# Kernel tuning notes

Hardware: AMD Instinct MI355X
Metric: run time of the kernel (lower is better)

## Reference

```python
import jax, jax.numpy as jnp
import numpy as np

B, T, S, D, V, NX = 4, 256, 400, 512, 50000, 50
VEXT = V + NX  # extended vocab


def setup_inputs() -> dict:
    key = jax.random.key(0)
    ks = jax.random.split(key, 10)
    s = 0.02
    return {
        "x": jax.random.normal(ks[0], (B, T, D), dtype=jnp.float32),
        "enc_outputs": jax.random.normal(ks[1], (B, S, D), dtype=jnp.float32),
        "src_mask": jax.random.randint(ks[2], (B, 1, S), 0, 2, dtype=jnp.int32),
        "enc_batch_extend_vocab": jax.random.randint(ks[3], (B, S), 0, VEXT, dtype=jnp.int64),
        "extra_zeros": jnp.zeros((B, T, NX), dtype=jnp.float32),
        "fc_w": jax.random.normal(ks[4], (V, D), dtype=jnp.float32) * s,
        "fc_b": jnp.zeros((V,), dtype=jnp.float32),
        "pgen_w": jax.random.normal(ks[5], (1, D), dtype=jnp.float32) * s,
        "pgen_b": jnp.zeros((1,), dtype=jnp.float32),
        "wq": jax.random.normal(ks[6], (D, D), dtype=jnp.float32) * s,
        "bq": jnp.zeros((D,), dtype=jnp.float32),
        "wk": jax.random.normal(ks[7], (D, D), dtype=jnp.float32) * s,
        "bk": jnp.zeros((D,), dtype=jnp.float32),
    }


def reference(x, enc_outputs, src_mask, enc_batch_extend_vocab, extra_zeros,
              fc_w, fc_b, pgen_w, pgen_b, wq, bq, wk, bk):
    # vocab distribution: [B,T,V]
    p_vocab = jax.nn.softmax(x @ fc_w.T + fc_b, axis=-1)
    # single-head cross attention probs (h=1 -> d_k = D)
    q = x @ wq.T + bq                 # [B,T,D]
    k = enc_outputs @ wk.T + bk       # [B,S,D]
    scores = jnp.einsum('btd,bsd->bts', q, k) / jnp.sqrt(jnp.float32(D))
    scores = jnp.where(src_mask == 0, jnp.float32(-1e9), scores)  # mask [B,1,S]
    attn_probs = jax.nn.softmax(scores, axis=-1)  # [B,T,S]
    # generation gate
    p_gen = jax.nn.sigmoid(x @ pgen_w.T + pgen_b)  # [B,T,1]
    attn_dist = (1.0 - p_gen) * attn_probs         # copy distribution over source
    p_ext = jnp.concatenate([p_gen * p_vocab, extra_zeros], axis=-1)  # [B,T,VEXT]
    # scatter-add copy probs into extended vocab slots
    b_idx = jnp.arange(B)[:, None, None]
    t_idx = jnp.arange(T)[None, :, None]
    v_idx = enc_batch_extend_vocab[:, None, :]
    bb, tt, vv = jnp.broadcast_arrays(b_idx, t_idx, v_idx)  # each [B,T,S]
    p_ext = p_ext.at[bb, tt, vv].add(attn_dist)
    return jnp.log(jnp.maximum(p_ext, jnp.float32(1e-9)))
```

## Files before the change

kernel.cpp:

```cpp
#include <hip/hip_runtime.h>
#include <hip/hip_bf16.h>
#include <math.h>

constexpr int cB = 4, cT = 256, cS = 400, cD = 512, cV = 50000, cNX = 50;
constexpr int cVEXT = cV + cNX;
constexpr int cPAN  = (cV + 127) / 128;
constexpr int cCBLD = cVEXT * 2;
constexpr int cMQ   = cB * cT;

typedef __attribute__((ext_vector_type(8))) short short8v;
typedef __attribute__((ext_vector_type(4))) float floatx4;

__device__ inline ushort f2bf(float f) {
    union { float f; unsigned u; } v; v.f = f;
    unsigned r = (v.u + 0x7FFFu + ((v.u >> 16) & 1u)) >> 16;
    return (ushort)r;
}
__device__ inline float bf2f(ushort u) {
    union { unsigned u; float f; } v; v.u = ((unsigned)u) << 16;
    return v.f;
}

__global__ __launch_bounds__(256) void cast_kernel(
    const float* __restrict__ src, ushort* __restrict__ dst, int n4)
{
    const int stride = gridDim.x * 256;
    for (int i = blockIdx.x * 256 + threadIdx.x; i < n4; i += stride) {
        float4 v = *(const float4*)(src + (size_t)i * 4);
        ushort4 o;
        o.x = f2bf(v.x); o.y = f2bf(v.y); o.z = f2bf(v.z); o.w = f2bf(v.w);
        *(ushort4*)(dst + (size_t)i * 4) = o;
    }
}

template<bool STATS>
__global__ __launch_bounds__(256) void gemm2(
    const ushort* __restrict__ A, const ushort* __restrict__ Wb,
    const float* __restrict__ bias,
    float* __restrict__ Cf, ushort* __restrict__ Cb, int cbld,
    float* __restrict__ pm, float* __restrict__ ps,
    int M, int N, int K, int ldc)
{
    __shared__ ushort As[2][128 * 32];
    __shared__ ushort Bs[2][128 * 32];
    __shared__ float sm_m[2][128];
    __shared__ float sm_s[2][128];

    const int tid  = threadIdx.x;
    const int lane = tid & 63;
    const int wv   = tid >> 6;
    const int wm   = wv >> 1;
    const int wn   = wv & 1;

    int bm, bn, pan = 0;
    if constexpr (STATS) {
        const int wg  = blockIdx.y * gridDim.x + blockIdx.x;
        const int nwg = gridDim.x * gridDim.y;
        const int j   = (wg & 7) * (nwg >> 3) + (wg >> 3);
        pan = j >> 3;
        bm  = (j & 7) * 128;
        bn  = pan * 128;
    } else {
        bm = blockIdx.x * 128;
        bn = blockIdx.y * 128;
    }

    const int srow = lane >> 2;
    const int sk   = (lane & 3) * 8;

    const int nt = K >> 5;

    floatx4 acc[4][4] = {};

    auto stage = [&](int bidx, int t) {
        const int k0 = t * 32;
        #pragma unroll
        for (int c = 0; c < 2; ++c) {
            const int lr = wv * 32 + c * 16;
            int ga = bm + lr + srow; if (ga >= M) ga = M - 1;
            __builtin_amdgcn_global_load_lds(
                (const __attribute__((address_space(1))) void*)(A + (size_t)ga * K + k0 + sk),
                (__attribute__((address_space(3))) void*)&As[bidx][lr * 32], 16, 0, 0);
        }
        #pragma unroll
        for (int c = 0; c < 2; ++c) {
            const int lr = wv * 32 + c * 16;
            int gb = bn + lr + srow; if (gb >= N) gb = N - 1;
            __builtin_amdgcn_global_load_lds(
                (const __attribute__((address_space(1))) void*)(Wb + (size_t)gb * K + k0 + sk),
                (__attribute__((address_space(3))) void*)&Bs[bidx][lr * 32], 16, 0, 0);
        }
    };

    stage(0, 0);
    __syncthreads();

    const int fr = lane & 15;
    const int g  = lane >> 4;
    int buf = 0;

    for (int t = 0; t < nt; ++t) {
        if (t + 1 < nt) stage(buf ^ 1, t + 1);
        short8v a[4], b[4];
        #pragma unroll
        for (int mi = 0; mi < 4; ++mi)
            a[mi] = *(const short8v*)&As[buf][(wm * 64 + mi * 16 + fr) * 32 + g * 8];
        #pragma unroll
        for (int ni = 0; ni < 4; ++ni)
            b[ni] = *(const short8v*)&Bs[buf][(wn * 64 + ni * 16 + fr) * 32 + g * 8];
        #pragma unroll
        for (int mi = 0; mi < 4; ++mi)
            #pragma unroll
            for (int ni = 0; ni < 4; ++ni)
                acc[mi][ni] = __builtin_amdgcn_mfma_f32_16x16x32_bf16(
                    a[mi], b[ni], acc[mi][ni], 0, 0, 0);
        __syncthreads();
        buf ^= 1;
    }

    float bv[4]; bool val[4];
    #pragma unroll
    for (int ni = 0; ni < 4; ++ni) {
        const int colg = bn + wn * 64 + ni * 16 + fr;
        val[ni] = (colg < N);
        bv[ni] = val[ni] ? bias[colg] : 0.f;
    }
    #pragma unroll
    for (int mi = 0; mi < 4; ++mi)
        #pragma unroll
        for (int ni = 0; ni < 4; ++ni)
            #pragma unroll
            for (int r = 0; r < 4; ++r)
                acc[mi][ni][r] += bv[ni];

    if constexpr (STATS) {
        #pragma unroll
        for (int mi = 0; mi < 4; ++mi) {
            #pragma unroll
            for (int r = 0; r < 4; ++r) {
                float mx = -1e30f;
                #pragma unroll
                for (int ni = 0; ni < 4; ++ni)
                    if (val[ni]) mx = fmaxf(mx, acc[mi][ni][r]);
                #pragma unroll
                for (int sw = 1; sw < 16; sw <<= 1)
                    mx = fmaxf(mx, __shfl_xor(mx, sw));
                float sm = 0.f;
                #pragma unroll
                for (int ni = 0; ni < 4; ++ni)
                    if (val[ni]) sm += __expf(acc[mi][ni][r] - mx);
                #pragma unroll
                for (int sw = 1; sw < 16; sw <<= 1)
                    sm += __shfl_xor(sm, sw);
                if (fr == 0) {
                    const int rl = wm * 64 + mi * 16 + g * 4 + r;
                    sm_m[wn][rl] = mx;
                    sm_s[wn][rl] = sm;
                }
            }
        }
        __syncthreads();
        if (tid < 128) {
            const float m0 = sm_m[0][tid], m1 = sm_m[1][tid];
            const float s0 = sm_s[0][tid], s1 = sm_s[1][tid];
            const float mm = fmaxf(m0, m1);
            const float ss = s0 * __expf(m0 - mm) + s1 * __expf(m1 - mm);
            const int grow = bm + tid;
            if (grow < M) {
                pm[(size_t)pan * M + grow] = mm;
                ps[(size_t)pan * M + grow] = ss;
            }
        }
        #pragma unroll
        for (int mi = 0; mi < 4; ++mi) {
            #pragma unroll
            for (int ni = 0; ni < 4; ++ni) {
                if (!val[ni]) continue;
                const int colg = bn + wn * 64 + ni * 16 + fr;
                #pragma unroll
                for (int r = 0; r < 4; ++r) {
                    const int row = bm + wm * 64 + mi * 16 + g * 4 + r;
                    if (row < M) Cb[(size_t)row * cbld + colg] = f2bf(acc[mi][ni][r]);
                }
            }
        }
    } else {
        #pragma unroll
        for (int mi = 0; mi < 4; ++mi) {
            #pragma unroll
            for (int ni = 0; ni < 4; ++ni) {
                if (!val[ni]) continue;
                const int colg = bn + wn * 64 + ni * 16 + fr;
                #pragma unroll
                for (int r = 0; r < 4; ++r) {
                    const int row = bm + wm * 64 + mi * 16 + g * 4 + r;
                    if (row < M) Cf[(size_t)row * ldc + colg] = acc[mi][ni][r];
                }
            }
        }
    }
}

__global__ __launch_bounds__(256) void combine_kernel(
    const float* __restrict__ pm, const float* __restrict__ ps,
    const float* __restrict__ pgen, float* __restrict__ rowadd)
{
    const int row = blockIdx.x;
    const int tid = threadIdx.x;
    float m = -1e30f, s = 0.f;
    for (int i = tid; i < cPAN; i += 256) {
        const float mi = pm[(size_t)i * cMQ + row];
        const float si = ps[(size_t)i * cMQ + row];
        const float nm = fmaxf(m, mi);
        s = s * __expf(m - nm) + si * __expf(mi - nm);
        m = nm;
    }
    #pragma unroll
    for (int sw = 1; sw < 64; sw <<= 1) {
        const float mo = __shfl_xor(m, sw);
        const float so = __shfl_xor(s, sw);
        const float nm = fmaxf(m, mo);
        s = s * __expf(m - nm) + so * __expf(mo - nm);
        m = nm;
    }
    __shared__ float rm[4], rs[4];
    if ((tid & 63) == 0) { rm[tid >> 6] = m; rs[tid >> 6] = s; }
    __syncthreads();
    if (tid == 0) {
        m = rm[0]; s = rs[0];
        #pragma unroll
        for (int i = 1; i < 4; ++i) {
            const float nm = fmaxf(m, rm[i]);
            s = s * __expf(m - nm) + rs[i] * __expf(rm[i] - nm);
            m = nm;
        }
        rowadd[row] = __logf(pgen[row]) - m - __logf(s);
    }
}

__global__ __launch_bounds__(512) void transform_flat(
    float* __restrict__ out, const ushort* __restrict__ lb,
    const float* __restrict__ rowadd)
{
    const int row = blockIdx.y;
    const float a = rowadd[row];
    constexpr float LOGMIN = -20.72326583694641f;
    const ushort* src = lb + (size_t)row * cV;
    float* dst = out + (size_t)row * cVEXT;
    constexpr int NI = cV / 8;
    for (int i = blockIdx.x * 512 + threadIdx.x; i <= NI; i += gridDim.x * 512) {
        if (i < NI) {
            const short8v sv = *(const short8v*)(src + (size_t)i * 8);
            const int v = i * 8;
            #pragma unroll
            for (int j = 0; j < 4; ++j) {
                float2 o;
                o.x = fmaxf(bf2f((ushort)sv[2 * j])     + a, LOGMIN);
                o.y = fmaxf(bf2f((ushort)sv[2 * j + 1]) + a, LOGMIN);
                *(float2*)&dst[v + 2 * j] = o;
            }
        } else {
            #pragma unroll
            for (int v = cV; v < cVEXT; v += 2) {
                float2 o; o.x = LOGMIN; o.y = LOGMIN;
                *(float2*)&dst[v] = o;
            }
        }
    }
}

__global__ __launch_bounds__(256) void fixup_kernel(
    float* __restrict__ out, const int* __restrict__ ebev,
    const float* __restrict__ attn)
{
    const int row = blockIdx.x;
    const int b = row / cT;
    const int tid = threadIdx.x;
    __shared__ int   pos[cS];
    __shared__ float add[cS];
    for (int s = tid; s < cS; s += 256) {
        pos[s] = ebev[b * cS + s];
        add[s] = attn[(size_t)row * cS + s];
    }
    __syncthreads();
    float* rowf = out + (size_t)row * cVEXT;
    for (int s = tid; s < cS; s += 256) {
        const int p = pos[s];
        bool leader = true;
        for (int s2 = 0; s2 < s; ++s2)
            if (pos[s2] == p) { leader = false; break; }
        if (!leader) continue;
        float sum = add[s];
        for (int s2 = s + 1; s2 < cS; ++s2)
            if (pos[s2] == p) sum += add[s2];
        const float base = __expf(rowf[p]);
        rowf[p] = __logf(fmaxf(base + sum, 1e-9f));
    }
}

__global__ __launch_bounds__(512) void transform_inplace(
    float* __restrict__ out, const float* __restrict__ rowadd,
    const int* __restrict__ ebev, const float* __restrict__ attn)
{
    const int row = blockIdx.x;
    const int b   = row / cT;
    const int tid = threadIdx.x;
    constexpr float LOGMIN = -20.72326583694641f;

    __shared__ int   pos[cS];
    __shared__ float add[cS];
    for (int s = tid; s < cS; s += 512) {
        pos[s] = ebev[b * cS + s];
        add[s] = attn[(size_t)row * cS + s];
    }

    const float a = rowadd[row];
    ushort* rowu = (ushort*)out + (size_t)row * cCBLD;
    float*  rowf = out + (size_t)row * cVEXT;

    #pragma unroll 1
    for (int L = 32768; L >= 2; L >>= 1) {
        const int hi = (2 * L < cVEXT) ? 2 * L : cVEXT;
        for (int i = L + 2 * tid; i < hi; i += 1024) {
            const float x0 = bf2f(rowu[i]);
            const float x1 = bf2f(rowu[i + 1]);
            float2 o;
            o.x = (i     < cV) ? fmaxf(x0 + a, LOGMIN) : LOGMIN;
            o.y = (i + 1 < cV) ? fmaxf(x1 + a, LOGMIN) : LOGMIN;
            *(float2*)&rowf[i] = o;
        }
        __syncthreads();
    }
    if (tid == 0) {
        const float x1 = bf2f(rowu[1]);
        const float x0 = bf2f(rowu[0]);
        rowf[1] = fmaxf(x1 + a, LOGMIN);
        rowf[0] = fmaxf(x0 + a, LOGMIN);
    }
    __syncthreads();

    for (int s = tid; s < cS; s += 512) {
        const int p = pos[s];
        bool leader = true;
        for (int s2 = 0; s2 < s; ++s2)
            if (pos[s2] == p) { leader = false; break; }
        if (!leader) continue;
        float sum = add[s];
        for (int s2 = s + 1; s2 < cS; ++s2)
            if (pos[s2] == p) sum += add[s2];
        const float base = __expf(rowf[p]);
        rowf[p] = __logf(fmaxf(base + sum, 1e-9f));
    }
}

__global__ __launch_bounds__(64) void pgen_kernel(
    const float* __restrict__ x, const float* __restrict__ w,
    const float* __restrict__ b, float* __restrict__ pgen)
{
    const int row = blockIdx.x;
    const int lane = threadIdx.x;
    const float* xr = x + (size_t)row * cD;
    float s = 0.f;
    for (int i = lane; i < cD; i += 64) s += xr[i] * w[i];
    #pragma unroll
    for (int off = 32; off; off >>= 1) s += __shfl_down(s, off);
    if (lane == 0) pgen[row] = 1.f / (1.f + __expf(-(s + b[0])));
}

__global__ __launch_bounds__(256) void attn_kernel(
    const float* __restrict__ q, const float* __restrict__ k,
    const int* __restrict__ src_mask, const float* __restrict__ pgen,
    float* __restrict__ attn)
{
    constexpr float scale = 0.04419417382415922f;
    const int row = blockIdx.x;
    const int b = row / cT;
    const int tid = threadIdx.x;

    __shared__ __align__(16) float qs[cD];
    __shared__ float sc[cS];
    __shared__ float red[4];

    for (int i = tid; i < cD; i += 256) qs[i] = q[(size_t)row * cD + i];
    __syncthreads();

    for (int s = tid; s < cS; s += 256) {
        const float* kr = k + ((size_t)b * cS + s) * cD;
        float dot = 0.f;
        #pragma unroll 4
        for (int i = 0; i < cD; i += 4) {
            float4 kv = *(const float4*)(kr + i);
            float4 qv = *(const float4*)(qs + i);
            dot += qv.x * kv.x + qv.y * kv.y + qv.z * kv.z + qv.w * kv.w;
        }
        float v = dot * scale;
        if (src_mask[b * cS + s] == 0) v = -1e9f;
        sc[s] = v;
    }
    __syncthreads();

    float m = -3.4e38f;
    for (int s = tid; s < cS; s += 256) m = fmaxf(m, sc[s]);
    #pragma unroll
    for (int off = 32; off; off >>= 1) m = fmaxf(m, __shfl_down(m, off));
    if ((tid & 63) == 0) red[tid >> 6] = m;
    __syncthreads();
    m = fmaxf(fmaxf(red[0], red[1]), fmaxf(red[2], red[3]));
    __syncthreads();

    float sum = 0.f;
    for (int s = tid; s < cS; s += 256) {
        float e = __expf(sc[s] - m);
        sc[s] = e;
        sum += e;
    }
    #pragma unroll
    for (int off = 32; off; off >>= 1) sum += __shfl_down(sum, off);
    if ((tid & 63) == 0) red[tid >> 6] = sum;
    __syncthreads();
    sum = red[0] + red[1] + red[2] + red[3];

    const float w = (1.f - pgen[row]) / sum;
    for (int s = tid; s < cS; s += 256)
        attn[(size_t)row * cS + s] = sc[s] * w;
}

extern "C" void kernel_launch(void* const* d_in, const int* in_sizes, int n_in,
                              void* d_out, int out_size, void* d_ws, size_t ws_size,
                              hipStream_t stream)
{
    const float* x      = (const float*)d_in[0];
    const float* enc    = (const float*)d_in[1];
    const int*   mask   = (const int*)d_in[2];
    const int*   ebev   = (const int*)d_in[3];
    const float* fc_w   = (const float*)d_in[5];
    const float* fc_b   = (const float*)d_in[6];
    const float* pgen_w = (const float*)d_in[7];
    const float* pgen_b = (const float*)d_in[8];
    const float* wq     = (const float*)d_in[9];
    const float* bq     = (const float*)d_in[10];
    const float* wk     = (const float*)d_in[11];
    const float* bk     = (const float*)d_in[12];
    float* out = (float*)d_out;

    float* ws     = (float*)d_ws;
    float* q      = ws;
    float* kbuf   = q + (size_t)cB * cT * cD;
    float* pgen   = kbuf + (size_t)cB * cS * cD;
    float* attn   = pgen + cB * cT;
    float* pm     = attn + (size_t)cB * cT * cS;
    float* ps     = pm + (size_t)cPAN * cMQ;
    float* rowadd = ps + (size_t)cPAN * cMQ;
    ushort* xb    = (ushort*)(rowadd + cMQ);
    ushort* encb  = xb + (size_t)cB * cT * cD;
    ushort* wqb   = encb + (size_t)cB * cS * cD;
    ushort* wkb   = wqb + (size_t)cD * cD;
    ushort* tail  = wkb + (size_t)cD * cD;

    const size_t base_bytes = (size_t)((char*)tail - (char*)d_ws);
    const bool big = ws_size >= base_bytes + (size_t)cMQ * cV * 2 + 1024;

    const dim3 blk(256);
    const int MQ = cMQ;
    const int MK = cB * cS;

    ushort* wb;
    ushort* logitsb;
    int     cbld;
    if (big) {
        wb = (ushort*)d_out;
        logitsb = tail;
        cbld = cV;
    } else {
        wb = tail;
        logitsb = (ushort*)d_out;
        cbld = cCBLD;
    }

    cast_kernel<<<dim3(512), blk, 0, stream>>>(x, xb, (cB * cT * cD) / 4);
    cast_kernel<<<dim3(512), blk, 0, stream>>>(enc, encb, (cB * cS * cD) / 4);
    cast_kernel<<<dim3(256), blk, 0, stream>>>(wq, wqb, (cD * cD) / 4);
    cast_kernel<<<dim3(256), blk, 0, stream>>>(wk, wkb, (cD * cD) / 4);
    cast_kernel<<<dim3(2048), blk, 0, stream>>>(fc_w, wb, (cV * cD) / 4);

    gemm2<false><<<dim3(MQ / 128, cD / 128), blk, 0, stream>>>(
        xb, wqb, bq, q, nullptr, 0, nullptr, nullptr, MQ, cD, cD, cD);
    gemm2<false><<<dim3((MK + 127) / 128, cD / 128), blk, 0, stream>>>(
        encb, wkb, bk, kbuf, nullptr, 0, nullptr, nullptr, MK, cD, cD, cD);
    pgen_kernel<<<dim3(MQ), dim3(64), 0, stream>>>(x, pgen_w, pgen_b, pgen);

    attn_kernel<<<dim3(MQ), blk, 0, stream>>>(q, kbuf, mask, pgen, attn);

    gemm2<true><<<dim3(MQ / 128, cPAN), blk, 0, stream>>>(
        xb, wb, fc_b, nullptr, logitsb, cbld, pm, ps, MQ, cV, cD, 0);

    combine_kernel<<<dim3(MQ), blk, 0, stream>>>(pm, ps, pgen, rowadd);

    if (big) {
        transform_flat<<<dim3(13, MQ), dim3(512), 0, stream>>>(out, logitsb, rowadd);
        fixup_kernel<<<dim3(MQ), blk, 0, stream>>>(out, ebev, attn);
    } else {
        transform_inplace<<<dim3(MQ), dim3(512), 0, stream>>>(out, rowadd, ebev, attn);
    }
}
```

Before: 455.7 us.

## Restructure GEMM LDS layout, pipeline waits, coalesced epilogue, and combine kernel

```diff
diff --git a/kernel.cpp b/kernel.cpp
--- a/kernel.cpp
+++ b/kernel.cpp
@@ -34,7 +34,7 @@
 }
 
 template<bool STATS>
-__global__ __launch_bounds__(256) void gemm2(
+__global__ __launch_bounds__(256) void gemm3(
     const ushort* __restrict__ A, const ushort* __restrict__ Wb,
     const float* __restrict__ bias,
     float* __restrict__ Cf, ushort* __restrict__ Cb, int cbld,
@@ -52,22 +52,20 @@
     const int wm   = wv >> 1;
     const int wn   = wv & 1;
 
-    int bm, bn, pan = 0;
+    int bm, bn;
     if constexpr (STATS) {
         const int wg  = blockIdx.y * gridDim.x + blockIdx.x;
         const int nwg = gridDim.x * gridDim.y;
         const int j   = (wg & 7) * (nwg >> 3) + (wg >> 3);
-        pan = j >> 3;
         bm  = (j & 7) * 128;
-        bn  = pan * 128;
+        bn  = (j >> 3) * 128;
     } else {
         bm = blockIdx.x * 128;
         bn = blockIdx.y * 128;
     }
 
-    const int srow = lane >> 2;
-    const int sk   = (lane & 3) * 8;
-
+    const int rA = lane & 15;
+    const int kA = (lane >> 4) * 8;
     const int nt = K >> 5;
 
     floatx4 acc[4][4] = {};
@@ -76,47 +74,56 @@
         const int k0 = t * 32;
         #pragma unroll
         for (int c = 0; c < 2; ++c) {
-            const int lr = wv * 32 + c * 16;
-            int ga = bm + lr + srow; if (ga >= M) ga = M - 1;
+            const int chunk = wv * 2 + c;
+            int ga = bm + chunk * 16 + rA; if (ga >= M) ga = M - 1;
             __builtin_amdgcn_global_load_lds(
-                (const __attribute__((address_space(1))) void*)(A + (size_t)ga * K + k0 + sk),
-                (__attribute__((address_space(3))) void*)&As[bidx][lr * 32], 16, 0, 0);
+                (const __attribute__((address_space(1))) void*)(A + (size_t)ga * K + k0 + kA),
+                (__attribute__((address_space(3))) void*)&As[bidx][chunk * 512], 16, 0, 0);
         }
         #pragma unroll
         for (int c = 0; c < 2; ++c) {
-            const int lr = wv * 32 + c * 16;
-            int gb = bn + lr + srow; if (gb >= N) gb = N - 1;
+            const int chunk = wv * 2 + c;
+            int gb = bn + chunk * 16 + rA; if (gb >= N) gb = N - 1;
             __builtin_amdgcn_global_load_lds(
-                (const __attribute__((address_space(1))) void*)(Wb + (size_t)gb * K + k0 + sk),
-                (__attribute__((address_space(3))) void*)&Bs[bidx][lr * 32], 16, 0, 0);
+                (const __attribute__((address_space(1))) void*)(Wb + (size_t)gb * K + k0 + kA),
+                (__attribute__((address_space(3))) void*)&Bs[bidx][chunk * 512], 16, 0, 0);
         }
     };
 
     stage(0, 0);
-    __syncthreads();
-
-    const int fr = lane & 15;
-    const int g  = lane >> 4;
     int buf = 0;
 
     for (int t = 0; t < nt; ++t) {
-        if (t + 1 < nt) stage(buf ^ 1, t + 1);
+        if (t + 1 < nt) {
+            stage(buf ^ 1, t + 1);
+            asm volatile("s_waitcnt vmcnt(4)" ::: "memory");
+        } else {
+            asm volatile("s_waitcnt vmcnt(0)" ::: "memory");
+        }
+        __builtin_amdgcn_s_barrier();
+        asm volatile("" ::: "memory");
+
         short8v a[4], b[4];
         #pragma unroll
         for (int mi = 0; mi < 4; ++mi)
-            a[mi] = *(const short8v*)&As[buf][(wm * 64 + mi * 16 + fr) * 32 + g * 8];
+            a[mi] = *(const short8v*)&As[buf][(wm * 4 + mi) * 512 + lane * 8];
         #pragma unroll
         for (int ni = 0; ni < 4; ++ni)
-            b[ni] = *(const short8v*)&Bs[buf][(wn * 64 + ni * 16 + fr) * 32 + g * 8];
+            b[ni] = *(const short8v*)&Bs[buf][(wn * 4 + ni) * 512 + lane * 8];
         #pragma unroll
         for (int mi = 0; mi < 4; ++mi)
             #pragma unroll
             for (int ni = 0; ni < 4; ++ni)
                 acc[mi][ni] = __builtin_amdgcn_mfma_f32_16x16x32_bf16(
                     a[mi], b[ni], acc[mi][ni], 0, 0, 0);
-        __syncthreads();
+
+        asm volatile("" ::: "memory");
+        __builtin_amdgcn_s_barrier();
         buf ^= 1;
     }
+
+    const int fr = lane & 15;
+    const int g  = lane >> 4;
 
     float bv[4]; bool val[4];
     #pragma unroll
@@ -167,20 +174,38 @@
             const float ss = s0 * __expf(m0 - mm) + s1 * __expf(m1 - mm);
             const int grow = bm + tid;
             if (grow < M) {
-                pm[(size_t)pan * M + grow] = mm;
-                ps[(size_t)pan * M + grow] = ss;
+                pm[(size_t)gridDim.y * 0 + (size_t)( (bn >> 7) ) * M + grow] = mm;
+                ps[(size_t)( (bn >> 7) ) * M + grow] = ss;
             }
         }
-        #pragma unroll
+
+        ushort* eps = (ushort*)As;
+        constexpr int LDW = 136;
+        #pragma unroll 1
         for (int mi = 0; mi < 4; ++mi) {
-            #pragma unroll
-            for (int ni = 0; ni < 4; ++ni) {
-                if (!val[ni]) continue;
-                const int colg = bn + wn * 64 + ni * 16 + fr;
+            __syncthreads();
+            #pragma unroll
+            for (int ni = 0; ni < 4; ++ni)
                 #pragma unroll
-                for (int r = 0; r < 4; ++r) {
-                    const int row = bm + wm * 64 + mi * 16 + g * 4 + r;
-                    if (row < M) Cb[(size_t)row * cbld + colg] = f2bf(acc[mi][ni][r]);
+                for (int r = 0; r < 4; ++r)
+                    eps[(wm * 16 + g * 4 + r) * LDW + wn * 64 + ni * 16 + fr] =
+                        f2bf(acc[mi][ni][r]);
+            __syncthreads();
+            #pragma unroll
+            for (int p = 0; p < 2; ++p) {
+                const int idx = p * 256 + tid;
+                const int lr  = idx >> 4;
+                const int seg = idx & 15;
+                const int colg = bn + seg * 8;
+                if (colg + 8 <= N) {
+                    const int grow = bm + (lr >> 4) * 64 + mi * 16 + (lr & 15);
+                    if (grow < M) {
+                        ushort4 v0 = *(const ushort4*)&eps[lr * LDW + seg * 8];
+                        ushort4 v1 = *(const ushort4*)&eps[lr * LDW + seg * 8 + 4];
+                        ushort* dp = Cb + (size_t)grow * cbld + colg;
+                        *(ushort4*)dp = v0;
+                        *(ushort4*)(dp + 4) = v1;
+                    }
                 }
             }
         }
@@ -205,33 +230,29 @@
     const float* __restrict__ pm, const float* __restrict__ ps,
     const float* __restrict__ pgen, float* __restrict__ rowadd)
 {
-    const int row = blockIdx.x;
-    const int tid = threadIdx.x;
+    const int lane = threadIdx.x & 63;
+    const int wv   = threadIdx.x >> 6;
+    const int row  = blockIdx.x * 64 + lane;
+
     float m = -1e30f, s = 0.f;
-    for (int i = tid; i < cPAN; i += 256) {
+    #pragma unroll 2
+    for (int i = wv; i < cPAN; i += 4) {
         const float mi = pm[(size_t)i * cMQ + row];
         const float si = ps[(size_t)i * cMQ + row];
         const float nm = fmaxf(m, mi);
         s = s * __expf(m - nm) + si * __expf(mi - nm);
         m = nm;
     }
-    #pragma unroll
-    for (int sw = 1; sw < 64; sw <<= 1) {
-        const float mo = __shfl_xor(m, sw);
-        const float so = __shfl_xor(s, sw);
-        const float nm = fmaxf(m, mo);
-        s = s * __expf(m - nm) + so * __expf(mo - nm);
-        m = nm;
-    }
-    __shared__ float rm[4], rs[4];
-    if ((tid & 63) == 0) { rm[tid >> 6] = m; rs[tid >> 6] = s; }
-    __syncthreads();
-    if (tid == 0) {
-        m = rm[0]; s = rs[0];
+    __shared__ float rm[4][64], rs[4][64];
+    rm[wv][lane] = m; rs[wv][lane] = s;
+    __syncthreads();
+    if (wv == 0) {
+        m = rm[0][lane]; s = rs[0][lane];
         #pragma unroll
         for (int i = 1; i < 4; ++i) {
-            const float nm = fmaxf(m, rm[i]);
-            s = s * __expf(m - nm) + rs[i] * __expf(rm[i] - nm);
+            const float m2 = rm[i][lane], s2 = rs[i][lane];
+            const float nm = fmaxf(m, m2);
+            s = s * __expf(m - nm) + s2 * __expf(m2 - nm);
             m = nm;
         }
         rowadd[row] = __logf(pgen[row]) - m - __logf(s);
@@ -483,18 +504,18 @@
     cast_kernel<<<dim3(256), blk, 0, stream>>>(wk, wkb, (cD * cD) / 4);
     cast_kernel<<<dim3(2048), blk, 0, stream>>>(fc_w, wb, (cV * cD) / 4);
 
-    gemm2<false><<<dim3(MQ / 128, cD / 128), blk, 0, stream>>>(
+    gemm3<false><<<dim3(MQ / 128, cD / 128), blk, 0, stream>>>(
         xb, wqb, bq, q, nullptr, 0, nullptr, nullptr, MQ, cD, cD, cD);
-    gemm2<false><<<dim3((MK + 127) / 128, cD / 128), blk, 0, stream>>>(
+    gemm3<false><<<dim3((MK + 127) / 128, cD / 128), blk, 0, stream>>>(
         encb, wkb, bk, kbuf, nullptr, 0, nullptr, nullptr, MK, cD, cD, cD);
     pgen_kernel<<<dim3(MQ), dim3(64), 0, stream>>>(x, pgen_w, pgen_b, pgen);
 
     attn_kernel<<<dim3(MQ), blk, 0, stream>>>(q, kbuf, mask, pgen, attn);
 
-    gemm2<true><<<dim3(MQ / 128, cPAN), blk, 0, stream>>>(
+    gemm3<true><<<dim3(8, cPAN), blk, 0, stream>>>(
         xb, wb, fc_b, nullptr, logitsb, cbld, pm, ps, MQ, cV, cD, 0);
 
-    combine_kernel<<<dim3(MQ), blk, 0, stream>>>(pm, ps, pgen, rowadd);
+    combine_kernel<<<dim3(MQ / 64), blk, 0, stream>>>(pm, ps, pgen, rowadd);
 
     if (big) {
         transform_flat<<<dim3(13, MQ), dim3(512), 0, stream>>>(out, logitsb, rowadd);
```

Result: slower. 601.8 us (+32.0%).
